# Optimization experiments

Hardware: AMD Instinct MI355X
Metric: run time of the kernel (lower is better)

The kernel has to match this reference:

```python
import jax, jax.numpy as jnp
import numpy as np
import math

D_MODEL = 1024
NUM_HEADS = 16
HEAD_DIM = D_MODEL // NUM_HEADS
THETA = 10000.0
B, S = 2, 2048


def _rope(x, positions, theta):
    # x: (b, h, s, d); positions: (s,) int
    d = x.shape[-1]
    inv_freq = theta ** (-jnp.arange(0, d, 2, dtype=jnp.float32) / d)  # (d/2,)
    ang = positions.astype(jnp.float32)[:, None] * inv_freq[None, :]   # (s, d/2)
    cos, sin = jnp.cos(ang), jnp.sin(ang)
    x1 = x[..., ::2]
    x2 = x[..., 1::2]
    r1 = x1 * cos - x2 * sin
    r2 = x1 * sin + x2 * cos
    # interleave back to (..., d)
    return jnp.stack([r1, r2], axis=-1).reshape(x.shape)


def setup_inputs() -> dict:
    key = jax.random.key(0)
    ks = jax.random.split(key, 5)
    std = math.sqrt(2.0 / (D_MODEL + D_MODEL))
    return {
        "x": jax.random.normal(ks[0], (B, S, D_MODEL), dtype=jnp.float32),
        "token_positions": jnp.arange(S, dtype=jnp.int32),
        "Wq": jax.random.normal(ks[1], (D_MODEL, D_MODEL), dtype=jnp.float32) * std,
        "Wk": jax.random.normal(ks[2], (D_MODEL, D_MODEL), dtype=jnp.float32) * std,
        "Wv": jax.random.normal(ks[3], (D_MODEL, D_MODEL), dtype=jnp.float32) * std,
        "Wo": jax.random.normal(ks[4], (D_MODEL, D_MODEL), dtype=jnp.float32) * std,
    }


def reference(x, token_positions, Wq, Wk, Wv, Wo):
    b, s, _ = x.shape
    def split_heads(t):
        return t.reshape(b, s, NUM_HEADS, HEAD_DIM).transpose(0, 2, 1, 3)  # (b,h,s,d)
    Q = split_heads(x @ Wq.T)
    K = split_heads(x @ Wk.T)
    V = split_heads(x @ Wv.T)
    Q = _rope(Q, token_positions, THETA)
    K = _rope(K, token_positions, THETA)
    scores = jnp.einsum("bhqd,bhkd->bhqk", Q, K) / math.sqrt(HEAD_DIM)
    causal = jnp.tril(jnp.ones((s, s), dtype=bool))
    scores = jnp.where(causal, scores, -jnp.inf)
    attn = jax.nn.softmax(scores, axis=-1)
    out = jnp.einsum("bhqk,bhkd->bhqd", attn, V)
    out = out.transpose(0, 2, 1, 3).reshape(b, s, D_MODEL)
    return out @ Wo.T
```

## Files before the change

### kernel.cpp

```cpp
#include <hip/hip_runtime.h>
#include <math.h>

typedef unsigned short u16;
typedef unsigned int   u32;
typedef __attribute__((ext_vector_type(8))) short bf16x8;
typedef __attribute__((ext_vector_type(4))) float floatx4;
typedef __attribute__((ext_vector_type(4))) _Float16 halfx4;
typedef __attribute__((ext_vector_type(2))) unsigned int uintx2;

#define SEQ 2048
#define DM  1024
#define NH  16
#define DH  64
#define MM  4096
#define QSCALE 0.18033688011112042f

__device__ __forceinline__ u16 f2bf(float f) {
    u32 u = __builtin_bit_cast(u32, f);
    u += 0x7fffu + ((u >> 16) & 1u);
    return (u16)(u >> 16);
}

__device__ __forceinline__ void async16(const void* g, void* l) {
    __builtin_amdgcn_global_load_lds(
        (const __attribute__((address_space(1))) void*)g,
        (__attribute__((address_space(3))) void*)l, 16, 0, 0);
}

__global__ __launch_bounds__(256) void prep_kernel(const float* __restrict__ x,
                                                   const float* __restrict__ w0,
                                                   const float* __restrict__ w1,
                                                   const float* __restrict__ w2,
                                                   const float* __restrict__ w3,
                                                   u16* __restrict__ Xsh,
                                                   u16* __restrict__ Wsh,
                                                   const int* __restrict__ pos,
                                                   float2* __restrict__ tab) {
    const int bid = blockIdx.x, cb = blockIdx.y, tid = threadIdx.x;

    int lin = bid * 16 + cb;
    if (lin < 256) {
        int i = lin * 256 + tid;
        int p = i >> 5, d2 = i & 31;
        float freq = __expf(-(float)d2 * (9.2103403719761836f / 32.0f));
        float sv, cv;
        sincosf((float)pos[p] * freq, &sv, &cv);
        tab[i] = make_float2(cv, sv);
    }

    const float* src; u16* dst; int row0;
    if (bid < 64) { src = x; dst = Xsh; row0 = bid * 64; }
    else {
        int wi = (bid - 64) >> 4;
        src = (wi == 0) ? w0 : (wi == 1) ? w1 : (wi == 2) ? w2 : w3;
        dst = Wsh + (size_t)wi * DM * DM;
        row0 = ((bid - 64) & 15) * 64;
    }
    __shared__ __align__(16) u16 t[64 * 64];
#pragma unroll
    for (int rep = 0; rep < 4; ++rep) {
        int f = rep * 256 + tid;
        int r = f >> 4, c4 = f & 15;
        float4 v = *(const float4*)&src[(size_t)(row0 + r) * DM + cb * 64 + c4 * 4];
        uint2 pk;
        pk.x = (u32)f2bf(v.x) | ((u32)f2bf(v.y) << 16);
        pk.y = (u32)f2bf(v.z) | ((u32)f2bf(v.w) << 16);
        int ch = (c4 >> 1) ^ (r & 7);
        *(uint2*)&t[r * 64 + ch * 8 + (c4 & 1) * 4] = pk;
    }
    __syncthreads();
#pragma unroll
    for (int rep = 0; rep < 2; ++rep) {
        int s = rep * 256 + tid;
        int tile = s >> 6, l = s & 63;
        int mt = tile >> 1, kt = tile & 1, lm = l & 15, quad = l >> 4;
        int m = mt * 16 + lm;
        uint4 v = *(const uint4*)&t[m * 64 + ((kt * 4 + quad) ^ (m & 7)) * 8];
        size_t rowblk = (size_t)(row0 >> 4) + mt;
        size_t ktile  = cb * 2 + kt;
        *(uint4*)&dst[(rowblk * 32 + ktile) * 512 + l * 8] = v;
    }
}

template<int NT, bool OUTF32>
__global__ __launch_bounds__(256) void gemm_nl(const u16* __restrict__ Ash,
                                               const u16* __restrict__ Wbase,
                                               u16* __restrict__ outbf,
                                               float* __restrict__ outf,
                                               _Float16* __restrict__ vtout,
                                               const float2* __restrict__ ropetab,
                                               int ropeMask) {
    const int z  = blockIdx.z;
    const u16* Wp = Wbase + (size_t)z * (DM * DM);
    const int m0 = blockIdx.x * 64, n0 = blockIdx.y * (NT * 64);
    const int tid  = threadIdx.x;
    const int lane = tid & 63, w = tid >> 6;
    const int lm = lane & 15, quad = lane >> 4;

    const u16* aB = Ash + ((size_t)(m0 >> 4) * 32) * 512 + lane * 8;
    const u16* bB = Wp  + ((size_t)((n0 >> 4) + w * NT) * 32) * 512 + lane * 8;

    floatx4 acc[4][NT];
    const floatx4 z4 = {0.f, 0.f, 0.f, 0.f};
#pragma unroll
    for (int mt = 0; mt < 4; ++mt)
#pragma unroll
        for (int nt = 0; nt < NT; ++nt) acc[mt][nt] = z4;

    bf16x8 ca[2][4], cb2[2][NT];
#pragma unroll
    for (int ks = 0; ks < 2; ++ks) {
#pragma unroll
        for (int mt = 0; mt < 4; ++mt)
            ca[ks][mt] = *(const bf16x8*)(aB + (size_t)mt * 16384 + ks * 512);
#pragma unroll
        for (int nt = 0; nt < NT; ++nt)
            cb2[ks][nt] = *(const bf16x8*)(bB + (size_t)nt * 16384 + ks * 512);
    }

#pragma unroll 2
    for (int it = 0; it < 16; ++it) {
        bf16x8 na[2][4], nb[2][NT];
        if (it < 15) {
            const size_t ko = (size_t)(it + 1) * 1024;
#pragma unroll
            for (int ks = 0; ks < 2; ++ks) {
#pragma unroll
                for (int mt = 0; mt < 4; ++mt)
                    na[ks][mt] = *(const bf16x8*)(aB + (size_t)mt * 16384 + ko + ks * 512);
#pragma unroll
                for (int nt = 0; nt < NT; ++nt)
                    nb[ks][nt] = *(const bf16x8*)(bB + (size_t)nt * 16384 + ko + ks * 512);
            }
        }
#pragma unroll
        for (int ks = 0; ks < 2; ++ks)
#pragma unroll
            for (int mt = 0; mt < 4; ++mt)
#pragma unroll
                for (int nt = 0; nt < NT; ++nt)
                    acc[mt][nt] = __builtin_amdgcn_mfma_f32_16x16x32_bf16(ca[ks][mt], cb2[ks][nt], acc[mt][nt], 0, 0, 0);
        if (it < 15) {
#pragma unroll
            for (int ks = 0; ks < 2; ++ks) {
#pragma unroll
                for (int mt = 0; mt < 4; ++mt) ca[ks][mt] = na[ks][mt];
#pragma unroll
                for (int nt = 0; nt < NT; ++nt) cb2[ks][nt] = nb[ks][nt];
            }
        }
    }

    if (!OUTF32 && z == 2) {
#pragma unroll
        for (int mt = 0; mt < 4; ++mt) {
            int row = m0 + mt * 16 + quad * 4;
            int b = row >> 11, s = row & (SEQ - 1);
#pragma unroll
            for (int nt = 0; nt < NT; ++nt) {
                int col = n0 + w * (NT * 16) + nt * 16 + lm;
                uint2 pk;
                pk.x = __builtin_bit_cast(u32, __builtin_amdgcn_cvt_pkrtz(acc[mt][nt][0], acc[mt][nt][1]));
                pk.y = __builtin_bit_cast(u32, __builtin_amdgcn_cvt_pkrtz(acc[mt][nt][2], acc[mt][nt][3]));
                *(uint2*)&vtout[((size_t)b * NH * DH + (size_t)col) * SEQ + s] = pk;
            }
        }
        return;
    }

    const bool rope = OUTF32 ? false : (((ropeMask >> z) & 1) != 0);
    const float osc = (!OUTF32 && z == 0) ? QSCALE : 1.0f;

#pragma unroll
    for (int mt = 0; mt < 4; ++mt)
#pragma unroll
        for (int r = 0; r < 4; ++r) {
            int row = m0 + mt * 16 + quad * 4 + r;
#pragma unroll
            for (int nt = 0; nt < NT; ++nt) {
                int col = n0 + w * (NT * 16) + nt * 16 + lm;
                float v  = acc[mt][nt][r];
                if (rope) {
                    float pv = __shfl_xor(v, 1);
                    float2 cs = ropetab[(row & (SEQ - 1)) * 32 + ((col & 63) >> 1)];
                    v = (lm & 1) ? fmaf(pv, cs.y, v * cs.x) : fmaf(v, cs.x, -pv * cs.y);
                }
                v *= osc;
                if (OUTF32) {
                    outf[(size_t)row * DM + col] = v;
                } else {
                    float hv = __shfl_xor(v, 1);
                    if (!(lm & 1)) {
                        u32 pk = (u32)f2bf(v) | ((u32)f2bf(hv) << 16);
                        *(u32*)&outbf[(size_t)z * ((size_t)MM * DM) + (size_t)row * DM + col] = pk;
                    }
                }
            }
        }
}

__global__ __launch_bounds__(512) void attn_kernel(const u16* __restrict__ Q,
                                                   const u16* __restrict__ K,
                                                   const _Float16* __restrict__ Vt,
                                                   u16* __restrict__ AO) {
    const int u  = blockIdx.x;
    const int qt = (u < 256) ? (15 - (u >> 5)) : ((u >> 5) - 8);
    const int bh = u & 31;
    const int b  = bh >> 4, h = bh & 15;
    const int q0 = qt * 128;
    const int tid = threadIdx.x, w = tid >> 6, lane = tid & 63;
    const int lm = lane & 15, quad = lane >> 4;

    __shared__ __align__(16) u16      lsK[2][128 * 64];
    __shared__ __align__(16) _Float16 lsV[2][64 * 128];

    bf16x8 qb[2];
#pragma unroll
    for (int ks = 0; ks < 2; ++ks)
        qb[ks] = *(const bf16x8*)
            &Q[(size_t)(b * SEQ + q0 + w * 16 + lm) * DM + h * DH + ks * 32 + quad * 8];

    const floatx4 z4 = {0.f, 0.f, 0.f, 0.f};
    floatx4 o[4];
#pragma unroll
    for (int dt = 0; dt < 4; ++dt) o[dt] = z4;
    float lsum = 0.f;

    const int qloc = w * 16 + lm;

    auto stageKV = [&](int buf, int kt) {
#pragma unroll
        for (int rep = 0; rep < 2; ++rep) {
            int f = rep * 512 + tid;
            int krow = f >> 3, kcb = (f & 7) ^ (krow & 7);
            async16(&K[(size_t)(b * SEQ + kt * 128 + krow) * DM + h * DH + kcb * 8],
                    &lsK[buf][f * 8]);
            int d = f >> 4, gbs = (f & 15) ^ ((d >> 1) & 7);
            async16(&Vt[(size_t)(bh * DH + d) * SEQ + kt * 128 + gbs * 8],
                    &lsV[buf][f * 8]);
        }
    };

    stageKV(0, 0);
    for (int kt = 0; kt <= qt; ++kt) {
        __syncthreads();
        if (kt < qt) stageKV((kt + 1) & 1, kt + 1);
        const u16*      Lk = lsK[kt & 1];
        const _Float16* Lv = lsV[kt & 1];

        floatx4 s4[8];
#pragma unroll
        for (int st = 0; st < 8; ++st) s4[st] = z4;
#pragma unroll
        for (int ks = 0; ks < 2; ++ks) {
            const int cbl = ((ks * 4 + quad) ^ (lm & 7)) * 8;
#pragma unroll
            for (int st = 0; st < 8; ++st) {
                bf16x8 ka = *(const bf16x8*)&Lk[(st * 16 + lm) * 64 + cbl];
                s4[st] = __builtin_amdgcn_mfma_f32_16x16x32_bf16(ka, qb[ks], s4[st], 0, 0, 0);
            }
        }

        halfx4 pb[8];
        const bool diag = (kt == qt);
#pragma unroll
        for (int st = 0; st < 8; ++st) {
#pragma unroll
            for (int r = 0; r < 4; ++r) {
                float v = s4[st][r];
                if (diag) {
                    int keyloc = st * 16 + quad * 4 + r;
                    if (keyloc > qloc) v = -1e30f;
                }
                v = exp2f(v);
                lsum += v;
                s4[st][r] = v;
            }
            uintx2 pk2;
            pk2.x = __builtin_bit_cast(u32, __builtin_amdgcn_cvt_pkrtz(s4[st][0], s4[st][1]));
            pk2.y = __builtin_bit_cast(u32, __builtin_amdgcn_cvt_pkrtz(s4[st][2], s4[st][3]));
            pb[st] = __builtin_bit_cast(halfx4, pk2);
        }

#pragma unroll
        for (int st = 0; st < 8; ++st) {
#pragma unroll
            for (int dt = 0; dt < 4; ++dt) {
                int drow = dt * 16 + lm;
                int sbs = (st * 2 + (quad >> 1)) ^ ((drow >> 1) & 7);
                halfx4 va = *(const halfx4*)&Lv[drow * 128 + sbs * 8 + (quad & 1) * 4];
                o[dt] = __builtin_amdgcn_mfma_f32_16x16x16f16(va, pb[st], o[dt], 0, 0, 0);
            }
        }
    }

    lsum += __shfl_xor(lsum, 16);
    lsum += __shfl_xor(lsum, 32);
    float rl = 1.0f / lsum;

    __syncthreads();
    u16* eb = (u16*)&lsK[0][0];
    const int q = w * 16 + lm;
#pragma unroll
    for (int dt = 0; dt < 4; ++dt) {
        uint2 pk;
        pk.x = (u32)f2bf(o[dt][0] * rl) | ((u32)f2bf(o[dt][1] * rl) << 16);
        pk.y = (u32)f2bf(o[dt][2] * rl) | ((u32)f2bf(o[dt][3] * rl) << 16);
        int ch = (dt * 2 + (quad >> 1)) ^ (lm & 7);
        *(uint2*)&eb[q * 64 + ch * 8 + (quad & 1) * 4] = pk;
    }
    __syncthreads();
    const size_t rowblk = (size_t)((b * SEQ + q0) >> 4) + w;
#pragma unroll
    for (int kt = 0; kt < 2; ++kt) {
        uint4 v = *(const uint4*)&eb[(w * 16 + lm) * 64 + ((kt * 4 + quad) ^ (lm & 7)) * 8];
        *(uint4*)&AO[(rowblk * 32 + (h * 2 + kt)) * 512 + lane * 8] = v;
    }
}

extern "C" void kernel_launch(void* const* d_in, const int* in_sizes, int n_in,
                              void* d_out, int out_size, void* d_ws, size_t ws_size,
                              hipStream_t stream) {
    const float* x   = (const float*)d_in[0];
    const int*   pos = (const int*)d_in[1];
    float* out = (float*)d_out;

    u16* ws = (u16*)d_ws;
    const size_t MD = (size_t)MM * DM;
    const size_t DD = (size_t)DM * DM;
    u16* Xsh = ws;
    u16* Wsh = ws + MD;
    u16* Qbf = ws + MD + 4 * DD;
    u16* Kbf = Qbf + MD;
    u16* VtB = Kbf + MD;
    float2* ropetab = (float2*)(VtB + MD);
    _Float16* Vt = (_Float16*)VtB;
    u16* AOsh = Xsh;

    prep_kernel<<<dim3(128, 16), 256, 0, stream>>>(
        x, (const float*)d_in[2], (const float*)d_in[3], (const float*)d_in[4],
        (const float*)d_in[5], Xsh, Wsh, pos, ropetab);

    gemm_nl<2, false><<<dim3(64, 8, 3), 256, 0, stream>>>(
        Xsh, Wsh, Qbf, nullptr, Vt, ropetab, 0x3);

    attn_kernel<<<dim3(512), 512, 0, stream>>>(Qbf, Kbf, Vt, AOsh);

    gemm_nl<2, true><<<dim3(64, 8, 1), 256, 0, stream>>>(
        AOsh, Wsh + 3 * DD, nullptr, out, nullptr, nullptr, 0);
}
```

Before: 195.7 us.

## Stage GEMM tiles through LDS with async loads and 128x128 block tiles

```diff
diff --git a/kernel.cpp b/kernel.cpp
--- a/kernel.cpp
+++ b/kernel.cpp
@@ -82,8 +82,8 @@
     }
 }
 
-template<int NT, bool OUTF32>
-__global__ __launch_bounds__(256) void gemm_nl(const u16* __restrict__ Ash,
+template<bool OUTF32>
+__global__ __launch_bounds__(256) void gemm_ls(const u16* __restrict__ Ash,
                                                const u16* __restrict__ Wbase,
                                                u16* __restrict__ outbf,
                                                float* __restrict__ outf,
@@ -92,73 +92,62 @@
                                                int ropeMask) {
     const int z  = blockIdx.z;
     const u16* Wp = Wbase + (size_t)z * (DM * DM);
-    const int m0 = blockIdx.x * 64, n0 = blockIdx.y * (NT * 64);
+    const int m0 = blockIdx.x * 128, n0 = blockIdx.y * 128;
     const int tid  = threadIdx.x;
     const int lane = tid & 63, w = tid >> 6;
+    const int wr = w >> 1, wc = w & 1;
     const int lm = lane & 15, quad = lane >> 4;
 
-    const u16* aB = Ash + ((size_t)(m0 >> 4) * 32) * 512 + lane * 8;
-    const u16* bB = Wp  + ((size_t)((n0 >> 4) + w * NT) * 32) * 512 + lane * 8;
-
-    floatx4 acc[4][NT];
+    __shared__ __align__(16) u16 lsA[16 * 512];
+    __shared__ __align__(16) u16 lsB[16 * 512];
+
+    const u16* aG = Ash + ((size_t)(m0 >> 4) * 32) * 512 + lane * 8;
+    const u16* bG = Wp  + ((size_t)(n0 >> 4) * 32) * 512 + lane * 8;
+
+    floatx4 acc[4][4];
     const floatx4 z4 = {0.f, 0.f, 0.f, 0.f};
 #pragma unroll
     for (int mt = 0; mt < 4; ++mt)
 #pragma unroll
-        for (int nt = 0; nt < NT; ++nt) acc[mt][nt] = z4;
-
-    bf16x8 ca[2][4], cb2[2][NT];
-#pragma unroll
-    for (int ks = 0; ks < 2; ++ks) {
-#pragma unroll
-        for (int mt = 0; mt < 4; ++mt)
-            ca[ks][mt] = *(const bf16x8*)(aB + (size_t)mt * 16384 + ks * 512);
-#pragma unroll
-        for (int nt = 0; nt < NT; ++nt)
-            cb2[ks][nt] = *(const bf16x8*)(bB + (size_t)nt * 16384 + ks * 512);
-    }
-
-#pragma unroll 2
+        for (int nt = 0; nt < 4; ++nt) acc[mt][nt] = z4;
+
     for (int it = 0; it < 16; ++it) {
-        bf16x8 na[2][4], nb[2][NT];
-        if (it < 15) {
-            const size_t ko = (size_t)(it + 1) * 1024;
-#pragma unroll
-            for (int ks = 0; ks < 2; ++ks) {
-#pragma unroll
-                for (int mt = 0; mt < 4; ++mt)
-                    na[ks][mt] = *(const bf16x8*)(aB + (size_t)mt * 16384 + ko + ks * 512);
-#pragma unroll
-                for (int nt = 0; nt < NT; ++nt)
-                    nb[ks][nt] = *(const bf16x8*)(bB + (size_t)nt * 16384 + ko + ks * 512);
-            }
-        }
+#pragma unroll
+        for (int rep = 0; rep < 4; ++rep) {
+            int c = w * 4 + rep;
+            int rb = c >> 1, kt = c & 1;
+            size_t go = ((size_t)rb * 32 + (size_t)it * 2 + kt) * 512;
+            async16(aG + go, &lsA[c * 512 + lane * 8]);
+            async16(bG + go, &lsB[c * 512 + lane * 8]);
+        }
+        __syncthreads();
+
+        bf16x8 ca[2][4], cb[2][4];
 #pragma unroll
         for (int ks = 0; ks < 2; ++ks)
 #pragma unroll
+            for (int t = 0; t < 4; ++t) {
+                ca[ks][t] = *(const bf16x8*)&lsA[((wr * 4 + t) * 2 + ks) * 512 + lane * 8];
+                cb[ks][t] = *(const bf16x8*)&lsB[((wc * 4 + t) * 2 + ks) * 512 + lane * 8];
+            }
+#pragma unroll
+        for (int ks = 0; ks < 2; ++ks)
+#pragma unroll
             for (int mt = 0; mt < 4; ++mt)
 #pragma unroll
-                for (int nt = 0; nt < NT; ++nt)
-                    acc[mt][nt] = __builtin_amdgcn_mfma_f32_16x16x32_bf16(ca[ks][mt], cb2[ks][nt], acc[mt][nt], 0, 0, 0);
-        if (it < 15) {
-#pragma unroll
-            for (int ks = 0; ks < 2; ++ks) {
-#pragma unroll
-                for (int mt = 0; mt < 4; ++mt) ca[ks][mt] = na[ks][mt];
-#pragma unroll
-                for (int nt = 0; nt < NT; ++nt) cb2[ks][nt] = nb[ks][nt];
-            }
-        }
+                for (int nt = 0; nt < 4; ++nt)
+                    acc[mt][nt] = __builtin_amdgcn_mfma_f32_16x16x32_bf16(ca[ks][mt], cb[ks][nt], acc[mt][nt], 0, 0, 0);
+        __syncthreads();
     }
 
     if (!OUTF32 && z == 2) {
 #pragma unroll
         for (int mt = 0; mt < 4; ++mt) {
-            int row = m0 + mt * 16 + quad * 4;
+            int row = m0 + wr * 64 + mt * 16 + quad * 4;
             int b = row >> 11, s = row & (SEQ - 1);
 #pragma unroll
-            for (int nt = 0; nt < NT; ++nt) {
-                int col = n0 + w * (NT * 16) + nt * 16 + lm;
+            for (int nt = 0; nt < 4; ++nt) {
+                int col = n0 + wc * 64 + nt * 16 + lm;
                 uint2 pk;
                 pk.x = __builtin_bit_cast(u32, __builtin_amdgcn_cvt_pkrtz(acc[mt][nt][0], acc[mt][nt][1]));
                 pk.y = __builtin_bit_cast(u32, __builtin_amdgcn_cvt_pkrtz(acc[mt][nt][2], acc[mt][nt][3]));
@@ -175,10 +164,10 @@
     for (int mt = 0; mt < 4; ++mt)
 #pragma unroll
         for (int r = 0; r < 4; ++r) {
-            int row = m0 + mt * 16 + quad * 4 + r;
-#pragma unroll
-            for (int nt = 0; nt < NT; ++nt) {
-                int col = n0 + w * (NT * 16) + nt * 16 + lm;
+            int row = m0 + wr * 64 + mt * 16 + quad * 4 + r;
+#pragma unroll
+            for (int nt = 0; nt < 4; ++nt) {
+                int col = n0 + wc * 64 + nt * 16 + lm;
                 float v  = acc[mt][nt][r];
                 if (rope) {
                     float pv = __shfl_xor(v, 1);
@@ -341,11 +330,11 @@
         x, (const float*)d_in[2], (const float*)d_in[3], (const float*)d_in[4],
         (const float*)d_in[5], Xsh, Wsh, pos, ropetab);
 
-    gemm_nl<2, false><<<dim3(64, 8, 3), 256, 0, stream>>>(
+    gemm_ls<false><<<dim3(32, 8, 3), 256, 0, stream>>>(
         Xsh, Wsh, Qbf, nullptr, Vt, ropetab, 0x3);
 
     attn_kernel<<<dim3(512), 512, 0, stream>>>(Qbf, Kbf, Vt, AOsh);
 
-    gemm_nl<2, true><<<dim3(64, 8, 1), 256, 0, stream>>>(
+    gemm_ls<true><<<dim3(32, 8, 1), 256, 0, stream>>>(
         AOsh, Wsh + 3 * DD, nullptr, out, nullptr, nullptr, 0);
 }
```

Measured after the change: 204.7 us. +4.6%, slower.
